# Kernel tuning notes

Hardware: AMD Instinct MI355X
Metric: run time of the kernel (lower is better)

## Reference

```python
import jax, jax.numpy as jnp
import numpy as np
from jax import lax


def setup_inputs() -> dict:
    key = jax.random.key(0)
    ks = jax.random.split(key, 8)
    N, L, I, H = 256, 512, 512, 1024
    s_i = 1.0 / np.sqrt(H)
    x = jax.random.normal(ks[0], (N, L, I), dtype=jnp.float32)
    h = jnp.zeros((N, H), dtype=jnp.float32)
    # GRUCell params (torch layout: weight_ih [3H, I], weight_hh [3H, H], gate order r,z,n)
    W_ih = jax.random.uniform(ks[1], (3 * H, I), dtype=jnp.float32, minval=-s_i, maxval=s_i)
    b_ih = jax.random.uniform(ks[2], (3 * H,), dtype=jnp.float32, minval=-s_i, maxval=s_i)
    W_hh = jax.random.uniform(ks[3], (3 * H, H), dtype=jnp.float32, minval=-s_i, maxval=s_i)
    b_hh = jax.random.uniform(ks[4], (3 * H,), dtype=jnp.float32, minval=-s_i, maxval=s_i)
    # fc_out: Linear(H, I)
    W_out = jax.random.uniform(ks[5], (I, H), dtype=jnp.float32, minval=-s_i, maxval=s_i)
    b_out = jax.random.uniform(ks[6], (I,), dtype=jnp.float32, minval=-s_i, maxval=s_i)
    return {"x": x, "h": h, "W_ih": W_ih, "b_ih": b_ih, "W_hh": W_hh, "b_hh": b_hh,
            "W_out": W_out, "b_out": b_out}


def reference(x, h, W_ih, b_ih, W_hh, b_hh, W_out, b_out):
    # Many-to-one GRU: scan GRUCell over time, linear head on final hidden state.
    def step(h, xt):
        gi = xt @ W_ih.T + b_ih          # [N, 3H]
        gh = h @ W_hh.T + b_hh           # [N, 3H]
        i_r, i_z, i_n = jnp.split(gi, 3, axis=-1)
        h_r, h_z, h_n = jnp.split(gh, 3, axis=-1)
        r = jax.nn.sigmoid(i_r + h_r)
        z = jax.nn.sigmoid(i_z + h_z)
        n = jnp.tanh(i_n + r * h_n)
        h_new = (1.0 - z) * n + z * h
        return h_new, None

    xs = jnp.swapaxes(x, 0, 1)           # [L, N, I] for scan over time
    h_final, _ = lax.scan(step, h, xs)
    y = h_final @ W_out.T + b_out        # [N, I]
    return (y, h_final)
```

## Files before the change

### kernel.cpp

```cpp
#include <hip/hip_runtime.h>


typedef unsigned short u16;
typedef unsigned int   u32;
typedef __attribute__((ext_vector_type(4))) float f32x4;
typedef __attribute__((ext_vector_type(8))) short s16x8;

constexpr int NB   = 256;
constexpr int LSEQ = 512;
constexpr int ISZ  = 512;
constexpr int HSZ  = 1024;

constexpr int TILE_U16  = 48 * 1536;
constexpr int TILEBYTES = TILE_U16 * 2;
constexpr int LDS_BYTES = 65536;

__device__ __forceinline__ u16 bf16_trunc(float f) {
    union { float f; u32 u; } v; v.f = f; return (u16)(v.u >> 16);
}
__device__ __forceinline__ float bf16_up(u16 h) {
    union { float f; u32 u; } v; v.u = ((u32)h) << 16; return v.f;
}
__device__ __forceinline__ u16 bf16_rtn(float f) {
    union { float f; u32 u; } v; v.f = f;
    u32 u = v.u; u += 0x7FFFu + ((u >> 16) & 1u);
    return (u16)(u >> 16);
}

#define MF(a, b, c) __builtin_amdgcn_mfma_f32_16x16x32_bf16(a, b, c, 0, 0, 0)

__global__ __launch_bounds__(256) void prep_kernel(
    const float* __restrict__ W_ih, const float* __restrict__ W_hh,
    const float* __restrict__ b_ih, const float* __restrict__ b_hh,
    const float* __restrict__ W_out,
    u16* __restrict__ Bhi, u16* __restrict__ Blo,
    float* __restrict__ Wt, float4* __restrict__ bias4)
{
    int idx = blockIdx.x * 256 + threadIdx.x;
    if (idx < 64 * TILE_U16) {
        int c   = idx / TILE_U16;
        int r1  = idx % TILE_U16;
        int kb  = r1 / 1536;
        int r2  = r1 % 1536;
        int p   = r2 / 512;
        int r3  = r2 % 512;
        int kg  = r3 >> 7;
        int col = (r3 >> 3) & 15;
        int e   = r3 & 7;
        int kloc = kg * 8 + e;
        int gcol = c * 16 + col;
        float w;
        if (kb < 16) w = W_ih[(p * HSZ + gcol) * ISZ + kb * 32 + kloc];
        else         w = W_hh[(p * HSZ + gcol) * HSZ + (kb - 16) * 32 + kloc];
        u16 hi = bf16_trunc(w);
        Bhi[idx] = hi;
        Blo[idx] = bf16_trunc(w - bf16_up(hi));
    }
    if (idx < HSZ * ISZ) {
        int i = idx % ISZ, k = idx / ISZ;
        Wt[idx] = W_out[i * HSZ + k];
    }
    if (idx < HSZ) {
        bias4[idx] = make_float4(b_ih[idx] + b_hh[idx],
                                 b_ih[HSZ + idx] + b_hh[HSZ + idx],
                                 b_ih[2 * HSZ + idx],
                                 b_hh[2 * HSZ + idx]);
    }
}

__global__ __launch_bounds__(256) void init_kernel(
    const float* __restrict__ x, const float* __restrict__ h_in,
    u16* __restrict__ xb0, float* __restrict__ hf0, u16* __restrict__ hb0)
{
    int idx = blockIdx.x * 256 + threadIdx.x;
    {
        int n = idx >> 9, k = idx & (ISZ - 1);
        xb0[idx] = bf16_rtn(x[(size_t)n * (LSEQ * ISZ) + k]);
    }
    #pragma unroll
    for (int q = 0; q < 2; ++q) {
        int e = idx * 2 + q;
        float v = h_in[e];
        hf0[e] = v;
        hb0[e] = bf16_rtn(v);
    }
}

__global__ __launch_bounds__(512, 1) void gru_step(
    const float* __restrict__ x, int t,
    const u16* __restrict__ Bhi, const u16* __restrict__ Blo,
    const float4* __restrict__ bias4,
    const u16* __restrict__ xb, u16* __restrict__ xb_n,
    float* __restrict__ hf,
    const u16* __restrict__ hb, u16* __restrict__ hb_n)
{
    extern __shared__ float scr[];

    const int tid  = threadIdx.x;
    const int lane = tid & 63;
    const int wv   = tid >> 6;
    const int lr   = lane & 15;
    const int kg   = lane >> 4;
    const int raw  = blockIdx.x;
    const int c    = ((raw & 7) << 3) | ((raw >> 3) & 7);
    const int m    = raw >> 6;
    const int fro  = kg * 128 + lr * 8;

    if (t + 1 < LSEQ) {
        int e = raw * 512 + tid;
        int n = e >> 9, k = e & (ISZ - 1);
        xb_n[e] = bf16_rtn(x[(size_t)n * (LSEQ * ISZ) + (size_t)(t + 1) * ISZ + k]);
    }

    const u16* bhit = Bhi + (size_t)c * TILE_U16;
    const u16* blot = Blo + (size_t)c * TILE_U16;

    f32x4 acc[4][4];
    #pragma unroll
    for (int rt = 0; rt < 4; ++rt)
        #pragma unroll
        for (int s = 0; s < 4; ++s) acc[rt][s] = (f32x4){0.f, 0.f, 0.f, 0.f};

    #pragma unroll 2
    for (int j = 0; j < 6; ++j) {
        const int kb = wv * 6 + j;
        const u16* gh = bhit + kb * 1536 + fro;
        const u16* gl = blot + kb * 1536 + fro;
        s16x8 bh0 = *(const s16x8*)gh;
        s16x8 bh1 = *(const s16x8*)(gh + 512);
        s16x8 bh2 = *(const s16x8*)(gh + 1024);
        s16x8 bl0 = *(const s16x8*)gl;
        s16x8 bl1 = *(const s16x8*)(gl + 512);
        s16x8 bl2 = *(const s16x8*)(gl + 1024);
        const bool isx = (kb < 16);
        s16x8 a[4];
        if (isx) {
            #pragma unroll
            for (int rt = 0; rt < 4; ++rt) {
                const int row = m * 64 + rt * 16 + lr;
                a[rt] = *(const s16x8*)(xb + row * ISZ + kb * 32 + kg * 8);
            }
        } else {
            #pragma unroll
            for (int rt = 0; rt < 4; ++rt) {
                const int row = m * 64 + rt * 16 + lr;
                a[rt] = *(const s16x8*)(hb + row * HSZ + (kb - 16) * 32 + kg * 8);
            }
        }
        #pragma unroll
        for (int rt = 0; rt < 4; ++rt) {
            acc[rt][0] = MF(a[rt], bh0, acc[rt][0]);
            acc[rt][0] = MF(a[rt], bl0, acc[rt][0]);
            acc[rt][1] = MF(a[rt], bh1, acc[rt][1]);
            acc[rt][1] = MF(a[rt], bl1, acc[rt][1]);
        }
        if (isx) {
            #pragma unroll
            for (int rt = 0; rt < 4; ++rt) {
                acc[rt][2] = MF(a[rt], bh2, acc[rt][2]);
                acc[rt][2] = MF(a[rt], bl2, acc[rt][2]);
            }
        } else {
            #pragma unroll
            for (int rt = 0; rt < 4; ++rt) {
                acc[rt][3] = MF(a[rt], bh2, acc[rt][3]);
                acc[rt][3] = MF(a[rt], bl2, acc[rt][3]);
            }
        }
    }

    if (wv >= 4) {
        float* sp = scr + (wv - 4) * 4096 + lane * 4;
        #pragma unroll
        for (int rt = 0; rt < 4; ++rt)
            #pragma unroll
            for (int s = 0; s < 4; ++s)
                *(f32x4*)(sp + (rt * 4 + s) * 256) = acc[rt][s];
    }
    __syncthreads();
    if (wv < 4) {
        const float* sp = scr + wv * 4096 + lane * 4;
        #pragma unroll
        for (int rt = 0; rt < 4; ++rt)
            #pragma unroll
            for (int s = 0; s < 4; ++s)
                acc[rt][s] += *(const f32x4*)(sp + (rt * 4 + s) * 256);
    }
    __syncthreads();
    if (wv == 2 || wv == 3) {
        float* sp = scr + (wv - 2) * 4096 + lane * 4;
        #pragma unroll
        for (int rt = 0; rt < 4; ++rt)
            #pragma unroll
            for (int s = 0; s < 4; ++s)
                *(f32x4*)(sp + (rt * 4 + s) * 256) = acc[rt][s];
    }
    __syncthreads();
    if (wv < 2) {
        const float* sp = scr + wv * 4096 + lane * 4;
        #pragma unroll
        for (int rt = 0; rt < 4; ++rt)
            #pragma unroll
            for (int s = 0; s < 4; ++s)
                acc[rt][s] += *(const f32x4*)(sp + (rt * 4 + s) * 256);
    }
    __syncthreads();
    if (wv == 1) {
        float* sp = scr + lane * 4;
        #pragma unroll
        for (int rt = 0; rt < 4; ++rt)
            #pragma unroll
            for (int s = 0; s < 4; ++s)
                *(f32x4*)(sp + (rt * 4 + s) * 256) = acc[rt][s];
    }
    __syncthreads();
    if (wv == 0) {
        const float* sp = scr + lane * 4;
        #pragma unroll
        for (int rt = 0; rt < 4; ++rt)
            #pragma unroll
            for (int s = 0; s < 4; ++s)
                acc[rt][s] += *(const f32x4*)(sp + (rt * 4 + s) * 256);
        const int j = c * 16 + lr;
        const float4 b4 = bias4[j];
        #pragma unroll
        for (int rt = 0; rt < 4; ++rt) {
            #pragma unroll
            for (int i = 0; i < 4; ++i) {
                const int row = m * 64 + rt * 16 + kg * 4 + i;
                float r_ = 1.f / (1.f + __expf(-(acc[rt][0][i] + b4.x)));
                float z_ = 1.f / (1.f + __expf(-(acc[rt][1][i] + b4.y)));
                float pre = (acc[rt][2][i] + b4.z) + r_ * (acc[rt][3][i] + b4.w);
                float e2 = __expf(2.f * pre);
                float ng = 1.f - 2.f / (e2 + 1.f);
                float ho = hf[row * HSZ + j];
                float hn = (1.f - z_) * ng + z_ * ho;
                hf[row * HSZ + j] = hn;
                hb_n[row * HSZ + j] = bf16_rtn(hn);
            }
        }
    }
}

__global__ __launch_bounds__(256) void head_kernel(
    const float* __restrict__ hfin, const float* __restrict__ Wt,
    const float* __restrict__ b_out, float* __restrict__ out)
{
    __shared__ float hrow[HSZ];
    const int n = blockIdx.x;
    const int tid = threadIdx.x;
    for (int k = tid; k < HSZ; k += 256) {
        float v = hfin[n * HSZ + k];
        hrow[k] = v;
        out[NB * ISZ + n * HSZ + k] = v;
    }
    __syncthreads();
    for (int j = tid; j < ISZ; j += 256) {
        float acc = b_out[j];
        #pragma unroll 8
        for (int k = 0; k < HSZ; ++k)
            acc = fmaf(hrow[k], Wt[k * ISZ + j], acc);
        out[n * ISZ + j] = acc;
    }
}

extern "C" void kernel_launch(void* const* d_in, const int* in_sizes, int n_in,
                              void* d_out, int out_size, void* d_ws, size_t ws_size,
                              hipStream_t stream) {
    (void)in_sizes; (void)n_in; (void)out_size; (void)ws_size;
    const float* x     = (const float*)d_in[0];
    const float* h_in  = (const float*)d_in[1];
    const float* W_ih  = (const float*)d_in[2];
    const float* b_ih  = (const float*)d_in[3];
    const float* W_hh  = (const float*)d_in[4];
    const float* b_hh  = (const float*)d_in[5];
    const float* W_out = (const float*)d_in[6];
    const float* b_out = (const float*)d_in[7];
    float* out = (float*)d_out;

    char* ws = (char*)d_ws;
    size_t o = 0;
    u16*    Bhi   = (u16*)(ws + o);    o += (size_t)64 * TILEBYTES;
    u16*    Blo   = (u16*)(ws + o);    o += (size_t)64 * TILEBYTES;
    float*  Wt    = (float*)(ws + o);  o += (size_t)HSZ * ISZ * 4;
    float4* bias4 = (float4*)(ws + o); o += (size_t)HSZ * 16;
    float*  hf    = (float*)(ws + o);  o += (size_t)NB * HSZ * 4;
    u16* hb[2]; u16* xb[2];
    for (int b = 0; b < 2; ++b) { hb[b] = (u16*)(ws + o); o += (size_t)NB * HSZ * 2; }
    for (int b = 0; b < 2; ++b) { xb[b] = (u16*)(ws + o); o += (size_t)NB * ISZ * 2; }

    prep_kernel<<<(64 * TILE_U16) / 256, 256, 0, stream>>>(
        W_ih, W_hh, b_ih, b_hh, W_out, Bhi, Blo, Wt, bias4);
    init_kernel<<<(NB * ISZ) / 256, 256, 0, stream>>>(
        x, h_in, xb[0], hf, hb[0]);

    for (int t = 0; t < LSEQ; ++t) {
        const int cur = t & 1, nxt = cur ^ 1;
        gru_step<<<256, 512, LDS_BYTES, stream>>>(
            x, t, Bhi, Blo, bias4,
            xb[cur], xb[nxt],
            hf, hb[cur], hb[nxt]);
    }
    head_kernel<<<NB, 256, 0, stream>>>(hf, Wt, b_out, out);
}
```

Measured before the change: 7.019 ms.

## Drop bf16 hi/lo weight split, use single rounded bf16 weights

Replaces the two-term bf16 (hi+lo) weight representation with a single round-to-nearest bf16 copy, halving MFMA count and weight loads per step. The final reduction stage is also split so waves 0 and 1 each finish and apply the gate math to half the row tiles, removing one LDS round trip and barrier. The cost is lower weight precision, which may increase error accumulated over the 512-step recurrence.

```diff
diff --git a/kernel.cpp b/kernel.cpp
--- a/kernel.cpp
+++ b/kernel.cpp
@@ -12,15 +12,8 @@
 constexpr int HSZ  = 1024;
 
 constexpr int TILE_U16  = 48 * 1536;
-constexpr int TILEBYTES = TILE_U16 * 2;
 constexpr int LDS_BYTES = 65536;
 
-__device__ __forceinline__ u16 bf16_trunc(float f) {
-    union { float f; u32 u; } v; v.f = f; return (u16)(v.u >> 16);
-}
-__device__ __forceinline__ float bf16_up(u16 h) {
-    union { float f; u32 u; } v; v.u = ((u32)h) << 16; return v.f;
-}
 __device__ __forceinline__ u16 bf16_rtn(float f) {
     union { float f; u32 u; } v; v.f = f;
     u32 u = v.u; u += 0x7FFFu + ((u >> 16) & 1u);
@@ -33,8 +26,7 @@
     const float* __restrict__ W_ih, const float* __restrict__ W_hh,
     const float* __restrict__ b_ih, const float* __restrict__ b_hh,
     const float* __restrict__ W_out,
-    u16* __restrict__ Bhi, u16* __restrict__ Blo,
-    float* __restrict__ Wt, float4* __restrict__ bias4)
+    u16* __restrict__ Bw, float* __restrict__ Wt, float4* __restrict__ bias4)
 {
     int idx = blockIdx.x * 256 + threadIdx.x;
     if (idx < 64 * TILE_U16) {
@@ -52,9 +44,7 @@
         float w;
         if (kb < 16) w = W_ih[(p * HSZ + gcol) * ISZ + kb * 32 + kloc];
         else         w = W_hh[(p * HSZ + gcol) * HSZ + (kb - 16) * 32 + kloc];
-        u16 hi = bf16_trunc(w);
-        Bhi[idx] = hi;
-        Blo[idx] = bf16_trunc(w - bf16_up(hi));
+        Bw[idx] = bf16_rtn(w);
     }
     if (idx < HSZ * ISZ) {
         int i = idx % ISZ, k = idx / ISZ;
@@ -88,8 +78,7 @@
 
 __global__ __launch_bounds__(512, 1) void gru_step(
     const float* __restrict__ x, int t,
-    const u16* __restrict__ Bhi, const u16* __restrict__ Blo,
-    const float4* __restrict__ bias4,
+    const u16* __restrict__ Bw, const float4* __restrict__ bias4,
     const u16* __restrict__ xb, u16* __restrict__ xb_n,
     float* __restrict__ hf,
     const u16* __restrict__ hb, u16* __restrict__ hb_n)
@@ -112,8 +101,7 @@
         xb_n[e] = bf16_rtn(x[(size_t)n * (LSEQ * ISZ) + (size_t)(t + 1) * ISZ + k]);
     }
 
-    const u16* bhit = Bhi + (size_t)c * TILE_U16;
-    const u16* blot = Blo + (size_t)c * TILE_U16;
+    const u16* bt = Bw + (size_t)c * TILE_U16;
 
     f32x4 acc[4][4];
     #pragma unroll
@@ -124,14 +112,10 @@
     #pragma unroll 2
     for (int j = 0; j < 6; ++j) {
         const int kb = wv * 6 + j;
-        const u16* gh = bhit + kb * 1536 + fro;
-        const u16* gl = blot + kb * 1536 + fro;
-        s16x8 bh0 = *(const s16x8*)gh;
-        s16x8 bh1 = *(const s16x8*)(gh + 512);
-        s16x8 bh2 = *(const s16x8*)(gh + 1024);
-        s16x8 bl0 = *(const s16x8*)gl;
-        s16x8 bl1 = *(const s16x8*)(gl + 512);
-        s16x8 bl2 = *(const s16x8*)(gl + 1024);
+        const u16* gh = bt + kb * 1536 + fro;
+        s16x8 b0 = *(const s16x8*)gh;
+        s16x8 b1 = *(const s16x8*)(gh + 512);
+        s16x8 b2 = *(const s16x8*)(gh + 1024);
         const bool isx = (kb < 16);
         s16x8 a[4];
         if (isx) {
@@ -149,23 +133,17 @@
         }
         #pragma unroll
         for (int rt = 0; rt < 4; ++rt) {
-            acc[rt][0] = MF(a[rt], bh0, acc[rt][0]);
-            acc[rt][0] = MF(a[rt], bl0, acc[rt][0]);
-            acc[rt][1] = MF(a[rt], bh1, acc[rt][1]);
-            acc[rt][1] = MF(a[rt], bl1, acc[rt][1]);
+            acc[rt][0] = MF(a[rt], b0, acc[rt][0]);
+            acc[rt][1] = MF(a[rt], b1, acc[rt][1]);
         }
         if (isx) {
             #pragma unroll
-            for (int rt = 0; rt < 4; ++rt) {
-                acc[rt][2] = MF(a[rt], bh2, acc[rt][2]);
-                acc[rt][2] = MF(a[rt], bl2, acc[rt][2]);
-            }
+            for (int rt = 0; rt < 4; ++rt)
+                acc[rt][2] = MF(a[rt], b2, acc[rt][2]);
         } else {
             #pragma unroll
-            for (int rt = 0; rt < 4; ++rt) {
-                acc[rt][3] = MF(a[rt], bh2, acc[rt][3]);
-                acc[rt][3] = MF(a[rt], bl2, acc[rt][3]);
-            }
+            for (int rt = 0; rt < 4; ++rt)
+                acc[rt][3] = MF(a[rt], b2, acc[rt][3]);
         }
     }
 
@@ -205,26 +183,35 @@
                 acc[rt][s] += *(const f32x4*)(sp + (rt * 4 + s) * 256);
     }
     __syncthreads();
-    if (wv == 1) {
+    if (wv == 0) {
         float* sp = scr + lane * 4;
         #pragma unroll
-        for (int rt = 0; rt < 4; ++rt)
-            #pragma unroll
-            for (int s = 0; s < 4; ++s)
-                *(f32x4*)(sp + (rt * 4 + s) * 256) = acc[rt][s];
-    }
-    __syncthreads();
-    if (wv == 0) {
-        const float* sp = scr + lane * 4;
-        #pragma unroll
-        for (int rt = 0; rt < 4; ++rt)
-            #pragma unroll
-            for (int s = 0; s < 4; ++s)
-                acc[rt][s] += *(const f32x4*)(sp + (rt * 4 + s) * 256);
+        for (int rr = 0; rr < 2; ++rr)
+            #pragma unroll
+            for (int s = 0; s < 4; ++s)
+                *(f32x4*)(sp + (rr * 4 + s) * 256) = acc[2 + rr][s];
+    } else if (wv == 1) {
+        float* sp = scr + 4096 + lane * 4;
+        #pragma unroll
+        for (int rr = 0; rr < 2; ++rr)
+            #pragma unroll
+            for (int s = 0; s < 4; ++s)
+                *(f32x4*)(sp + (rr * 4 + s) * 256) = acc[rr][s];
+    }
+    __syncthreads();
+    if (wv < 2) {
+        const int rt0 = (wv == 0) ? 0 : 2;
+        const float* sp = scr + (1 - wv) * 4096 + lane * 4;
+        #pragma unroll
+        for (int rr = 0; rr < 2; ++rr)
+            #pragma unroll
+            for (int s = 0; s < 4; ++s)
+                acc[rt0 + rr][s] += *(const f32x4*)(sp + (rr * 4 + s) * 256);
         const int j = c * 16 + lr;
         const float4 b4 = bias4[j];
         #pragma unroll
-        for (int rt = 0; rt < 4; ++rt) {
+        for (int rr = 0; rr < 2; ++rr) {
+            const int rt = rt0 + rr;
             #pragma unroll
             for (int i = 0; i < 4; ++i) {
                 const int row = m * 64 + rt * 16 + kg * 4 + i;
@@ -280,8 +267,7 @@
 
     char* ws = (char*)d_ws;
     size_t o = 0;
-    u16*    Bhi   = (u16*)(ws + o);    o += (size_t)64 * TILEBYTES;
-    u16*    Blo   = (u16*)(ws + o);    o += (size_t)64 * TILEBYTES;
+    u16*    Bw    = (u16*)(ws + o);    o += (size_t)64 * TILE_U16 * 2;
     float*  Wt    = (float*)(ws + o);  o += (size_t)HSZ * ISZ * 4;
     float4* bias4 = (float4*)(ws + o); o += (size_t)HSZ * 16;
     float*  hf    = (float*)(ws + o);  o += (size_t)NB * HSZ * 4;
@@ -290,14 +276,14 @@
     for (int b = 0; b < 2; ++b) { xb[b] = (u16*)(ws + o); o += (size_t)NB * ISZ * 2; }
 
     prep_kernel<<<(64 * TILE_U16) / 256, 256, 0, stream>>>(
-        W_ih, W_hh, b_ih, b_hh, W_out, Bhi, Blo, Wt, bias4);
+        W_ih, W_hh, b_ih, b_hh, W_out, Bw, Wt, bias4);
     init_kernel<<<(NB * ISZ) / 256, 256, 0, stream>>>(
         x, h_in, xb[0], hf, hb[0]);
 
     for (int t = 0; t < LSEQ; ++t) {
         const int cur = t & 1, nxt = cur ^ 1;
         gru_step<<<256, 512, LDS_BYTES, stream>>>(
-            x, t, Bhi, Blo, bias4,
+            x, t, Bw, bias4,
             xb[cur], xb[nxt],
             hf, hb[cur], hb[nxt]);
     }
```

After: 14.51 ms. 2.07x slower.
